# Kernel tuning notes

Hardware: AMD Instinct MI355X
Metric: run time of the kernel (lower is better)

Reference implementation:

```python
import jax, jax.numpy as jnp
import numpy as np

N_EMBD = 512
N_HEADS = 8
N_KV_HEADS = 2
HEAD_DIM = N_EMBD // N_HEADS  # 64
ROPE_BASE = 1000000.0
B, T = 2, 4096


def _rotate_half(x):
    h = x.shape[-1] // 2
    return jnp.concatenate([-x[..., h:], x[..., :h]], axis=-1)


def _build_rope(head_dim, seq_len, base, dtype):
    inv_freq = 1.0 / base ** (jnp.arange(0, head_dim, 2, dtype=jnp.float32) / head_dim)
    t = jnp.arange(seq_len, dtype=jnp.float32)
    freqs = jnp.outer(t, inv_freq)            # [T, head_dim/2]
    emb = jnp.concatenate([freqs, freqs], axis=-1)  # [T, head_dim]
    return emb.astype(dtype), None  # placeholder, cos/sin computed by caller


def setup_inputs() -> dict:
    key = jax.random.key(0)
    ks = jax.random.split(key, 8)
    s_in = 1.0 / np.sqrt(N_EMBD)
    x = jax.random.normal(ks[0], (B, T, N_EMBD), dtype=jnp.float32)
    Wq = jax.random.normal(ks[1], (N_EMBD, N_HEADS * HEAD_DIM), dtype=jnp.float32) * s_in
    bq = jnp.zeros((N_HEADS * HEAD_DIM,), dtype=jnp.float32)
    Wk = jax.random.normal(ks[2], (N_EMBD, N_KV_HEADS * HEAD_DIM), dtype=jnp.float32) * s_in
    bk = jnp.zeros((N_KV_HEADS * HEAD_DIM,), dtype=jnp.float32)
    Wv = jax.random.normal(ks[3], (N_EMBD, N_KV_HEADS * HEAD_DIM), dtype=jnp.float32) * s_in
    bv = jnp.zeros((N_KV_HEADS * HEAD_DIM,), dtype=jnp.float32)
    Wo = jax.random.normal(ks[4], (N_HEADS * HEAD_DIM, N_EMBD), dtype=jnp.float32) * s_in
    return {"x": x, "Wq": Wq, "bq": bq, "Wk": Wk, "bk": bk, "Wv": Wv, "bv": bv, "Wo": Wo}


def reference(x, Wq, bq, Wk, bk, Wv, bv, Wo):
    Bx, Tx, _ = x.shape
    scale = HEAD_DIM ** -0.5
    q = (x @ Wq + bq).reshape(Bx, Tx, N_HEADS, HEAD_DIM).transpose(0, 2, 1, 3)      # [B,H,T,D]
    k = (x @ Wk + bk).reshape(Bx, Tx, N_KV_HEADS, HEAD_DIM).transpose(0, 2, 1, 3)   # [B,Hkv,T,D]
    v = (x @ Wv + bv).reshape(Bx, Tx, N_KV_HEADS, HEAD_DIM).transpose(0, 2, 1, 3)

    # RoPE (built in fp32 then cast, matching torch impl)
    inv_freq = 1.0 / ROPE_BASE ** (jnp.arange(0, HEAD_DIM, 2, dtype=jnp.float32) / HEAD_DIM)
    t = jnp.arange(Tx, dtype=jnp.float32)
    freqs = jnp.outer(t, inv_freq)
    emb = jnp.concatenate([freqs, freqs], axis=-1)          # [T, D]
    cos = jnp.cos(emb).astype(x.dtype)[None, None, :, :]    # broadcast over B,H
    sin = jnp.sin(emb).astype(x.dtype)[None, None, :, :]
    q = q * cos + _rotate_half(q) * sin
    k = k * cos + _rotate_half(k) * sin

    rep = N_HEADS // N_KV_HEADS
    k = jnp.repeat(k, rep, axis=1)   # repeat_interleave on head dim
    v = jnp.repeat(v, rep, axis=1)

    attn = jnp.einsum("bhtd,bhsd->bhts", q, k) * scale      # [B,H,T,T]
    causal = jnp.tril(jnp.ones((Tx, Tx), dtype=bool))
    attn = jnp.where(causal, attn, jnp.finfo(attn.dtype).min)
    attn = jax.nn.softmax(attn, axis=-1)
    out = jnp.einsum("bhts,bhsd->bhtd", attn, v)            # [B,H,T,D]
    out = out.transpose(0, 2, 1, 3).reshape(Bx, Tx, N_HEADS * HEAD_DIM)
    return out @ Wo
```

## Files before the change

### kernel.cpp

```cpp
#include <hip/hip_runtime.h>

typedef unsigned short u16;
typedef unsigned int u32;
typedef __bf16 bf16x8_t __attribute__((ext_vector_type(8)));
typedef float f32x4_t __attribute__((ext_vector_type(4)));
typedef float f32x16_t __attribute__((ext_vector_type(16)));

#define T_SEQ 4096
#define EMB 512
#define NH 8
#define NKV 2
#define HD 64

__device__ __forceinline__ float bf2f(u16 h) {
    union { unsigned u; float f; } x; x.u = ((unsigned)h) << 16; return x.f;
}
__device__ __forceinline__ u16 f2bf(float f) {
    union { float f; unsigned u; } x; x.f = f;
    unsigned r = x.u + 0x7FFFu + ((x.u >> 16) & 1u);
    return (u16)(r >> 16);
}

__global__ __launch_bounds__(256)
void prep_kernel(const float* __restrict__ Wq, const float* __restrict__ Wk,
                 const float* __restrict__ Wv, const float* __restrict__ Wo,
                 u16* __restrict__ WqkvT, u16* __restrict__ WoT,
                 float* __restrict__ cost, float* __restrict__ sint)
{
    int i = blockIdx.x * 256 + threadIdx.x;
    if (i < 262144) {
        int n = i >> 9, k = i & 511;
        WqkvT[i] = f2bf(Wq[(size_t)k * 512 + n]);
    } else if (i < 327680) {
        int j = i - 262144;
        int n = j >> 9, k = j & 511;
        WqkvT[i] = f2bf(Wk[(size_t)k * 128 + n]);
    } else if (i < 393216) {
        int j = i - 327680;
        int n = j >> 9, k = j & 511;
        WqkvT[i] = f2bf(Wv[(size_t)k * 128 + n]);
    } else if (i < 655360) {
        int j = i - 393216;
        int n = j >> 9, k = j & 511;
        WoT[j] = f2bf(Wo[(size_t)k * 512 + n]);
    } else {
        int j = i - 655360;
        int t = j >> 5, jj = j & 31;
        double invf = pow(1.0e6, -(double)jj / 32.0);
        double ang = (double)t * invf;
        cost[j] = (float)cos(ang);
        sint[j] = (float)sin(ang);
    }
}

template <int EPI, int ASRC>
__global__ __launch_bounds__(256)
void gemm_kernel(const u16* __restrict__ A, const float* __restrict__ Af32,
                 const u16* __restrict__ Bt, int K,
                 float* __restrict__ C, int N,
                 const float* __restrict__ bq, const float* __restrict__ bk,
                 const float* __restrict__ bv,
                 const float* __restrict__ cost, const float* __restrict__ sint,
                 u16* __restrict__ qw, u16* __restrict__ kw, u16* __restrict__ vt)
{
    __shared__ __align__(16) u16 As[64][72];
    __shared__ __align__(16) u16 Bs[128][72];

    const int tid  = threadIdx.x;
    const int lane = tid & 63, wave = tid >> 6;
    const int wr = wave >> 1, wc = wave & 1;
    const int tm = blockIdx.x, tn = blockIdx.y;
    const int lrow = lane & 15, lgrp = lane >> 4;

    f32x4_t acc[2][4];
#pragma unroll
    for (int i = 0; i < 2; ++i)
#pragma unroll
        for (int j = 0; j < 4; ++j) acc[i][j] = (f32x4_t){0.f, 0.f, 0.f, 0.f};

    for (int k0 = 0; k0 < K; k0 += 64) {
        __syncthreads();
        {
            const int r0 = tid >> 3;
            const int ko = (tid & 7) * 8;
#pragma unroll
            for (int rr = 0; rr < 2; ++rr) {
                int row = r0 + rr * 32;
                int grow = tm * 64 + row;
                if (ASRC == 0) {
                    uint4 va = *reinterpret_cast<const uint4*>(A + (size_t)grow * K + k0 + ko);
                    *reinterpret_cast<uint4*>(&As[row][ko]) = va;
                } else {
                    float4 f0 = *reinterpret_cast<const float4*>(Af32 + (size_t)grow * K + k0 + ko);
                    float4 f1 = *reinterpret_cast<const float4*>(Af32 + (size_t)grow * K + k0 + ko + 4);
                    u16 o[8] = { f2bf(f0.x), f2bf(f0.y), f2bf(f0.z), f2bf(f0.w),
                                 f2bf(f1.x), f2bf(f1.y), f2bf(f1.z), f2bf(f1.w) };
                    *reinterpret_cast<uint4*>(&As[row][ko]) = *reinterpret_cast<uint4*>(o);
                }
            }
#pragma unroll
            for (int rr = 0; rr < 4; ++rr) {
                int row = r0 + rr * 32;
                uint4 vb = *reinterpret_cast<const uint4*>(Bt + (size_t)(tn * 128 + row) * K + k0 + ko);
                *reinterpret_cast<uint4*>(&Bs[row][ko]) = vb;
            }
        }
        __syncthreads();
#pragma unroll
        for (int kc = 0; kc < 2; ++kc) {
            bf16x8_t af[2], bf[4];
#pragma unroll
            for (int mb = 0; mb < 2; ++mb)
                af[mb] = *reinterpret_cast<const bf16x8_t*>(&As[wr * 32 + mb * 16 + lrow][kc * 32 + lgrp * 8]);
#pragma unroll
            for (int nb = 0; nb < 4; ++nb)
                bf[nb] = *reinterpret_cast<const bf16x8_t*>(&Bs[wc * 64 + nb * 16 + lrow][kc * 32 + lgrp * 8]);
#pragma unroll
            for (int mb = 0; mb < 2; ++mb)
#pragma unroll
                for (int nb = 0; nb < 4; ++nb)
                    acc[mb][nb] = __builtin_amdgcn_mfma_f32_16x16x32_bf16(af[mb], bf[nb], acc[mb][nb], 0, 0, 0);
        }
    }

    if (EPI == 0) {
#pragma unroll
        for (int mb = 0; mb < 2; ++mb)
#pragma unroll
            for (int nb = 0; nb < 4; ++nb)
#pragma unroll
                for (int r = 0; r < 4; ++r) {
                    int row = tm * 64 + wr * 32 + mb * 16 + lgrp * 4 + r;
                    int col = tn * 128 + wc * 64 + nb * 16 + lrow;
                    C[(size_t)row * N + col] = acc[mb][nb][r];
                }
    } else {
        const float QSC = 0.125f * 1.44269504088896f;
#pragma unroll
        for (int mb = 0; mb < 2; ++mb)
#pragma unroll
            for (int r = 0; r < 4; ++r) {
                int grow = tm * 64 + wr * 32 + mb * 16 + lgrp * 4 + r;
                int b = grow >> 12, t = grow & 4095;
#pragma unroll
                for (int nb = 0; nb < 2; ++nb) {
                    int n = tn * 128 + wc * 64 + nb * 16 + lrow;
                    int j = n & 63;
                    float c0 = acc[mb][nb][r];
                    float c1 = acc[mb][nb + 2][r];
                    if (n < 512) {
                        c0 += bq[n]; c1 += bq[n + 32];
                        float cs = cost[t * 32 + j], sn = sint[t * 32 + j];
                        float r0 = (c0 * cs - c1 * sn) * QSC;
                        float r1 = (c1 * cs + c0 * sn) * QSC;
                        int h = n >> 6;
                        size_t base = ((size_t)(b * NH + h) * T_SEQ + t) * HD;
                        qw[base + j]      = f2bf(r0);
                        qw[base + j + 32] = f2bf(r1);
                    } else if (n < 640) {
                        int nn = n - 512;
                        c0 += bk[nn]; c1 += bk[nn + 32];
                        float cs = cost[t * 32 + j], sn = sint[t * 32 + j];
                        float r0 = c0 * cs - c1 * sn;
                        float r1 = c1 * cs + c0 * sn;
                        int hk2 = nn >> 6;
                        size_t base = ((size_t)(b * NKV + hk2) * T_SEQ + t) * HD;
                        kw[base + j]      = f2bf(r0);
                        kw[base + j + 32] = f2bf(r1);
                    } else {
                        int nn = n - 640;
                        c0 += bv[nn]; c1 += bv[nn + 32];
                        int hv = nn >> 6;
                        size_t base = (size_t)(b * NKV + hv) * HD * T_SEQ;
                        vt[base + (size_t)j * T_SEQ + t]        = f2bf(c0);
                        vt[base + (size_t)(j + 32) * T_SEQ + t] = f2bf(c1);
                    }
                }
            }
    }
}

__global__ __launch_bounds__(256)
void attn_kernel(const u16* __restrict__ qw, const u16* __restrict__ kw,
                 const u16* __restrict__ vt, u16* __restrict__ po, float* __restrict__ lb)
{
    __shared__ __align__(16) u16 Ks[2][64][64];
    __shared__ __align__(16) u16 Vs[2][64][64];

    const int hdix = blockIdx.x;
    const int b = hdix >> 3, h = hdix & 7, hk = h >> 2;
    const int qt = 31 - (int)blockIdx.y;
    const int ck = blockIdx.z;
    const int tid = threadIdx.x, lane = tid & 63, wave = tid >> 6;
    const int lid = lane & 31, hi = lane >> 5;
    const int q0 = qt * 128 + wave * 32;
    const int kt0 = ck * (qt + 1);
    const int kt1 = kt0 + (qt + 1);

    const u16* kbase  = kw + (size_t)(b * NKV + hk) * T_SEQ * HD;
    const u16* vtbase = vt + (size_t)(b * NKV + hk) * HD * T_SEQ;

    const int ss = tid >> 3;
    const int sg = tid & 7;
    const int swz = (sg ^ (ss & 7)) << 3;

    bf16x8_t qf[4];
    {
        const u16* qrow = qw + ((size_t)(b * NH + h) * T_SEQ + q0 + lid) * HD + 8 * hi;
#pragma unroll
        for (int t = 0; t < 4; ++t)
            qf[t] = *reinterpret_cast<const bf16x8_t*>(qrow + 16 * t);
    }

    f32x16_t o0, o1, z16;
#pragma unroll
    for (int i = 0; i < 16; ++i) { o0[i] = 0.f; o1[i] = 0.f; z16[i] = 0.f; }
    const float M_FIX = 16.0f;
    float l = 0.f;

    {
        const int s2 = kt0 * 64;
        uint4 ka  = *reinterpret_cast<const uint4*>(kbase + (size_t)(s2 + ss) * HD + sg * 8);
        uint4 kb2 = *reinterpret_cast<const uint4*>(kbase + (size_t)(s2 + ss + 32) * HD + sg * 8);
        uint4 va  = *reinterpret_cast<const uint4*>(vtbase + (size_t)ss * T_SEQ + s2 + sg * 8);
        uint4 vb2 = *reinterpret_cast<const uint4*>(vtbase + (size_t)(ss + 32) * T_SEQ + s2 + sg * 8);
        *reinterpret_cast<uint4*>(&Ks[0][ss][swz]) = ka;
        *reinterpret_cast<uint4*>(&Ks[0][ss + 32][swz]) = kb2;
        *reinterpret_cast<uint4*>(&Vs[0][ss][swz]) = va;
        *reinterpret_cast<uint4*>(&Vs[0][ss + 32][swz]) = vb2;
    }
    __syncthreads();

    for (int kt = kt0; kt < kt1; ++kt) {
        const int cur = (kt - kt0) & 1, nxt = cur ^ 1;
        const bool pre = (kt + 1 < kt1);

        uint4 kr0, kr1, vr0, vr1;
        if (pre) {
            const int s2 = (kt + 1) * 64;
            kr0 = *reinterpret_cast<const uint4*>(kbase + (size_t)(s2 + ss) * HD + sg * 8);
            kr1 = *reinterpret_cast<const uint4*>(kbase + (size_t)(s2 + ss + 32) * HD + sg * 8);
            vr0 = *reinterpret_cast<const uint4*>(vtbase + (size_t)ss * T_SEQ + s2 + sg * 8);
            vr1 = *reinterpret_cast<const uint4*>(vtbase + (size_t)(ss + 32) * T_SEQ + s2 + sg * 8);
        }

        if (kt * 64 <= q0 + 31) {
            const bool full = (kt * 64 + 32 <= q0 + 31);
            const bool mreq = (kt * 64 + 63 > q0);

            f32x16_t s0, s1;
            __builtin_amdgcn_s_setprio(1);
#pragma unroll
            for (int t = 0; t < 4; ++t) {
                const int g = ((2 * t + hi) ^ (lid & 7)) << 3;
                bf16x8_t ka = *reinterpret_cast<const bf16x8_t*>(&Ks[cur][lid][g]);
                s0 = __builtin_amdgcn_mfma_f32_32x32x16_bf16(ka, qf[t], (t == 0) ? z16 : s0, 0, 0, 0);
                if (full) {
                    bf16x8_t kb2 = *reinterpret_cast<const bf16x8_t*>(&Ks[cur][lid + 32][g]);
                    s1 = __builtin_amdgcn_mfma_f32_32x32x16_bf16(kb2, qf[t], (t == 0) ? z16 : s1, 0, 0, 0);
                }
            }
            __builtin_amdgcn_s_setprio(0);

            if (mreq) {
                const int qg = q0 + lid;
                const int kvb = kt * 64 + 4 * hi;
#pragma unroll
                for (int r = 0; r < 16; ++r) {
                    int kv = kvb + (r & 3) + 8 * (r >> 2);
                    if (kv > qg) s0[r] = -1e30f;
                    if (full && kv + 32 > qg) s1[r] = -1e30f;
                }
            }

#pragma unroll
            for (int r = 0; r < 16; ++r) s0[r] = exp2f(s0[r] - M_FIX);
            if (full) {
#pragma unroll
                for (int r = 0; r < 16; ++r) s1[r] = exp2f(s1[r] - M_FIX);
            }

            {
                float rs = 0.f;
#pragma unroll
                for (int q4 = 0; q4 < 4; ++q4)
                    rs += (s0[4 * q4] + s0[4 * q4 + 1]) + (s0[4 * q4 + 2] + s0[4 * q4 + 3]);
                if (full) {
#pragma unroll
                    for (int q4 = 0; q4 < 4; ++q4)
                        rs += (s1[4 * q4] + s1[4 * q4 + 1]) + (s1[4 * q4 + 2] + s1[4 * q4 + 3]);
                }
                rs += __shfl_xor(rs, 32);
                l += rs;
            }

            bf16x8_t pa[4];
            {
                u32 pw[8];
#pragma unroll
                for (int c = 0; c < 4; ++c) {
                    asm("v_cvt_pk_bf16_f32 %0, %1, %2" : "=v"(pw[2 * c])     : "v"(s0[4 * c]),     "v"(s0[4 * c + 1]));
                    asm("v_cvt_pk_bf16_f32 %0, %1, %2" : "=v"(pw[2 * c + 1]) : "v"(s0[4 * c + 2]), "v"(s0[4 * c + 3]));
                }
                asm("v_permlane32_swap_b32 %0, %1" : "+v"(pw[0]), "+v"(pw[2]));
                asm("v_permlane32_swap_b32 %0, %1" : "+v"(pw[1]), "+v"(pw[3]));
                asm("v_permlane32_swap_b32 %0, %1" : "+v"(pw[4]), "+v"(pw[6]));
                asm("v_permlane32_swap_b32 %0, %1" : "+v"(pw[5]), "+v"(pw[7]));
                uint4 f0 = {pw[0], pw[1], pw[2], pw[3]};
                uint4 f1 = {pw[4], pw[5], pw[6], pw[7]};
                pa[0] = __builtin_bit_cast(bf16x8_t, f0);
                pa[1] = __builtin_bit_cast(bf16x8_t, f1);
                if (full) {
#pragma unroll
                    for (int c = 0; c < 4; ++c) {
                        asm("v_cvt_pk_bf16_f32 %0, %1, %2" : "=v"(pw[2 * c])     : "v"(s1[4 * c]),     "v"(s1[4 * c + 1]));
                        asm("v_cvt_pk_bf16_f32 %0, %1, %2" : "=v"(pw[2 * c + 1]) : "v"(s1[4 * c + 2]), "v"(s1[4 * c + 3]));
                    }
                    asm("v_permlane32_swap_b32 %0, %1" : "+v"(pw[0]), "+v"(pw[2]));
                    asm("v_permlane32_swap_b32 %0, %1" : "+v"(pw[1]), "+v"(pw[3]));
                    asm("v_permlane32_swap_b32 %0, %1" : "+v"(pw[4]), "+v"(pw[6]));
                    asm("v_permlane32_swap_b32 %0, %1" : "+v"(pw[5]), "+v"(pw[7]));
                    uint4 g0 = {pw[0], pw[1], pw[2], pw[3]};
                    uint4 g1 = {pw[4], pw[5], pw[6], pw[7]};
                    pa[2] = __builtin_bit_cast(bf16x8_t, g0);
                    pa[3] = __builtin_bit_cast(bf16x8_t, g1);
                }
            }

            __builtin_amdgcn_s_setprio(1);
            const int ns = full ? 4 : 2;
#pragma unroll
            for (int s = 0; s < 4; ++s) {
                if (s >= ns) break;
                const int g = ((2 * s + hi) ^ (lid & 7)) << 3;
                bf16x8_t v0f = *reinterpret_cast<const bf16x8_t*>(&Vs[cur][lid][g]);
                bf16x8_t v1f = *reinterpret_cast<const bf16x8_t*>(&Vs[cur][lid + 32][g]);
                o0 = __builtin_amdgcn_mfma_f32_32x32x16_bf16(pa[s], v0f, o0, 0, 0, 0);
                o1 = __builtin_amdgcn_mfma_f32_32x32x16_bf16(pa[s], v1f, o1, 0, 0, 0);
            }
            __builtin_amdgcn_s_setprio(0);
        }

        if (pre) {
            *reinterpret_cast<uint4*>(&Ks[nxt][ss][swz]) = kr0;
            *reinterpret_cast<uint4*>(&Ks[nxt][ss + 32][swz]) = kr1;
            *reinterpret_cast<uint4*>(&Vs[nxt][ss][swz]) = vr0;
            *reinterpret_cast<uint4*>(&Vs[nxt][ss + 32][swz]) = vr1;
            __syncthreads();
        }
    }

    {
        u16* pob = po + (size_t)ck * 4194304;
        const int rowb = (hdix * 32 + qt) * 128;
#pragma unroll
        for (int r = 0; r < 16; ++r) {
            int qr = (r & 3) + 8 * (r >> 2) + 4 * hi;
            size_t base = (size_t)(rowb + wave * 32 + qr) * HD;
            pob[base + lid]      = f2bf(o0[r]);
            pob[base + lid + 32] = f2bf(o1[r]);
        }
        if (hi == 0)
            lb[(size_t)ck * 65536 + rowb + wave * 32 + lid] = l;
    }
}

__global__ __launch_bounds__(256)
void combine_kernel(const u16* __restrict__ po, const float* __restrict__ lb,
                    u16* __restrict__ ao)
{
    int id = blockIdx.x * 256 + threadIdx.x;
    int row = id >> 3, oct = id & 7;
    int bhqt = row >> 7, qrow = row & 127;
    int bh = bhqt >> 5, qt = bhqt & 31;
    int b = bh >> 3, h = bh & 7;
    int t = qt * 128 + qrow;

    float inv = 1.0f / (lb[row] + lb[65536 + row]);
    const u16* p0 = po + (size_t)row * HD + oct * 8;
    const u16* p1 = p0 + 4194304;
    uint4 a = *reinterpret_cast<const uint4*>(p0);
    uint4 c = *reinterpret_cast<const uint4*>(p1);
    const u16* pa = reinterpret_cast<const u16*>(&a);
    const u16* pc = reinterpret_cast<const u16*>(&c);
    u16 outv[8];
#pragma unroll
    for (int j = 0; j < 8; ++j)
        outv[j] = f2bf((bf2f(pa[j]) + bf2f(pc[j])) * inv);
    size_t base = ((size_t)(b * T_SEQ) + t) * EMB + h * HD + oct * 8;
    *reinterpret_cast<uint2*>(ao + base)     = *reinterpret_cast<uint2*>(&outv[0]);
    *reinterpret_cast<uint2*>(ao + base + 4) = *reinterpret_cast<uint2*>(&outv[4]);
}

extern "C" void kernel_launch(void* const* d_in, const int* in_sizes, int n_in,
                              void* d_out, int out_size, void* d_ws, size_t ws_size,
                              hipStream_t stream)
{
    const float* x  = (const float*)d_in[0];
    const float* Wq = (const float*)d_in[1];
    const float* bq = (const float*)d_in[2];
    const float* Wk = (const float*)d_in[3];
    const float* bk = (const float*)d_in[4];
    const float* Wv = (const float*)d_in[5];
    const float* bv = (const float*)d_in[6];
    const float* Wo = (const float*)d_in[7];
    float* out = (float*)d_out;

    char* ws = (char*)d_ws;
    u16*   WqkvT = (u16*)(ws);
    u16*   WoT   = (u16*)(ws + 786432);
    float* cost  = (float*)(ws + 1310720);
    float* sint  = (float*)(ws + 1835008);
    u16*   qw    = (u16*)(ws + 10747904);
    u16*   kw    = (u16*)(ws + 19136512);
    u16*   vt    = (u16*)(ws + 21233664);
    u16*   ao    = (u16*)(ws + 23330816);
    u16*   po    = (u16*)(ws + 31719424);
    float* lb    = (float*)(ws + 48496640);

    prep_kernel<<<3072, 256, 0, stream>>>(Wq, Wk, Wv, Wo, WqkvT, WoT, cost, sint);

    dim3 gp(128, 6);
    gemm_kernel<1, 1><<<gp, 256, 0, stream>>>(nullptr, x, WqkvT, 512,
                                              nullptr, 768,
                                              bq, bk, bv, cost, sint, qw, kw, vt);

    dim3 ga(2 * NH, 32, 2);
    attn_kernel<<<ga, 256, 0, stream>>>(qw, kw, vt, po, lb);

    combine_kernel<<<65536 * 8 / 256, 256, 0, stream>>>(po, lb, ao);

    dim3 go(128, 4);
    gemm_kernel<0, 0><<<go, 256, 0, stream>>>(ao, nullptr, WoT, 512,
                                              out, 512,
                                              nullptr, nullptr, nullptr, nullptr, nullptr,
                                              nullptr, nullptr, nullptr);
}
```

Before: 130.7 us.

## Fuse split-K attention combine into attention kernel via atomic last-block reduction

Removes the separate combine kernel. Each attention block now bumps an atomic counter for its query tile, and the second of the two key-split blocks to finish merges the other block's partial output and normalizer with its own register accumulators, then writes the final bf16 output. The grid is also flattened to 1D so the two splits of a tile sit next to each other in launch order. This saves one kernel launch and a round trip of reading the partial outputs, at the cost of threadfences and an atomic per block, plus counters that are zeroed in the prep kernel.

```diff
diff --git a/kernel.cpp b/kernel.cpp
--- a/kernel.cpp
+++ b/kernel.cpp
@@ -25,7 +25,7 @@
 void prep_kernel(const float* __restrict__ Wq, const float* __restrict__ Wk,
                  const float* __restrict__ Wv, const float* __restrict__ Wo,
                  u16* __restrict__ WqkvT, u16* __restrict__ WoT,
-                 float* __restrict__ cost, float* __restrict__ sint)
+                 float* __restrict__ cost, float* __restrict__ sint, int* __restrict__ cnt)
 {
     int i = blockIdx.x * 256 + threadIdx.x;
     if (i < 262144) {
@@ -43,13 +43,15 @@
         int j = i - 393216;
         int n = j >> 9, k = j & 511;
         WoT[j] = f2bf(Wo[(size_t)k * 512 + n]);
-    } else {
+    } else if (i < 786432) {
         int j = i - 655360;
         int t = j >> 5, jj = j & 31;
         double invf = pow(1.0e6, -(double)jj / 32.0);
         double ang = (double)t * invf;
         cost[j] = (float)cos(ang);
         sint[j] = (float)sin(ang);
+    } else {
+        cnt[i - 786432] = 0;
     }
 }
 
@@ -182,15 +184,18 @@
 
 __global__ __launch_bounds__(256)
 void attn_kernel(const u16* __restrict__ qw, const u16* __restrict__ kw,
-                 const u16* __restrict__ vt, u16* __restrict__ po, float* __restrict__ lb)
+                 const u16* __restrict__ vt, u16* __restrict__ po, float* __restrict__ lb,
+                 int* __restrict__ cnt, u16* __restrict__ ao)
 {
     __shared__ __align__(16) u16 Ks[2][64][64];
     __shared__ __align__(16) u16 Vs[2][64][64];
-
-    const int hdix = blockIdx.x;
+    __shared__ int flag;
+
+    const int gid = blockIdx.x;
+    const int hdix = gid & 15;
+    const int ck = (gid >> 4) & 1;
+    const int qt = 31 - (gid >> 5);
     const int b = hdix >> 3, h = hdix & 7, hk = h >> 2;
-    const int qt = 31 - (int)blockIdx.y;
-    const int ck = blockIdx.z;
     const int tid = threadIdx.x, lane = tid & 63, wave = tid >> 6;
     const int lid = lane & 31, hi = lane >> 5;
     const int q0 = qt * 128 + wave * 32;
@@ -350,9 +355,9 @@
         }
     }
 
+    const int rowb = (hdix * 32 + qt) * 128;
     {
         u16* pob = po + (size_t)ck * 4194304;
-        const int rowb = (hdix * 32 + qt) * 128;
 #pragma unroll
         for (int r = 0; r < 16; ++r) {
             int qr = (r & 3) + 8 * (r >> 2) + 4 * hi;
@@ -363,33 +368,26 @@
         if (hi == 0)
             lb[(size_t)ck * 65536 + rowb + wave * 32 + lid] = l;
     }
-}
-
-__global__ __launch_bounds__(256)
-void combine_kernel(const u16* __restrict__ po, const float* __restrict__ lb,
-                    u16* __restrict__ ao)
-{
-    int id = blockIdx.x * 256 + threadIdx.x;
-    int row = id >> 3, oct = id & 7;
-    int bhqt = row >> 7, qrow = row & 127;
-    int bh = bhqt >> 5, qt = bhqt & 31;
-    int b = bh >> 3, h = bh & 7;
-    int t = qt * 128 + qrow;
-
-    float inv = 1.0f / (lb[row] + lb[65536 + row]);
-    const u16* p0 = po + (size_t)row * HD + oct * 8;
-    const u16* p1 = p0 + 4194304;
-    uint4 a = *reinterpret_cast<const uint4*>(p0);
-    uint4 c = *reinterpret_cast<const uint4*>(p1);
-    const u16* pa = reinterpret_cast<const u16*>(&a);
-    const u16* pc = reinterpret_cast<const u16*>(&c);
-    u16 outv[8];
-#pragma unroll
-    for (int j = 0; j < 8; ++j)
-        outv[j] = f2bf((bf2f(pa[j]) + bf2f(pc[j])) * inv);
-    size_t base = ((size_t)(b * T_SEQ) + t) * EMB + h * HD + oct * 8;
-    *reinterpret_cast<uint2*>(ao + base)     = *reinterpret_cast<uint2*>(&outv[0]);
-    *reinterpret_cast<uint2*>(ao + base + 4) = *reinterpret_cast<uint2*>(&outv[4]);
+    __threadfence();
+    if (tid == 0) flag = atomicAdd(&cnt[hdix * 32 + qt], 1);
+    __syncthreads();
+    if (flag == 1) {
+        __threadfence();
+        const int ock = ck ^ 1;
+        const u16* pob2 = po + (size_t)ock * 4194304;
+        float lo = lb[(size_t)ock * 65536 + rowb + wave * 32 + lid];
+        float inv = 1.0f / (l + lo);
+#pragma unroll
+        for (int r = 0; r < 16; ++r) {
+            int qr = (r & 3) + 8 * (r >> 2) + 4 * hi;
+            float ir = __shfl(inv, qr);
+            size_t pbase = (size_t)(rowb + wave * 32 + qr) * HD;
+            int t = qt * 128 + wave * 32 + qr;
+            size_t abase = ((size_t)(b * T_SEQ) + t) * EMB + h * HD;
+            ao[abase + lid]      = f2bf((o0[r] + bf2f(pob2[pbase + lid]))      * ir);
+            ao[abase + lid + 32] = f2bf((o1[r] + bf2f(pob2[pbase + lid + 32])) * ir);
+        }
+    }
 }
 
 extern "C" void kernel_launch(void* const* d_in, const int* in_sizes, int n_in,
@@ -417,18 +415,16 @@
     u16*   ao    = (u16*)(ws + 23330816);
     u16*   po    = (u16*)(ws + 31719424);
     float* lb    = (float*)(ws + 48496640);
-
-    prep_kernel<<<3072, 256, 0, stream>>>(Wq, Wk, Wv, Wo, WqkvT, WoT, cost, sint);
+    int*   cnt   = (int*)(ws + 49020928);
+
+    prep_kernel<<<3074, 256, 0, stream>>>(Wq, Wk, Wv, Wo, WqkvT, WoT, cost, sint, cnt);
 
     dim3 gp(128, 6);
     gemm_kernel<1, 1><<<gp, 256, 0, stream>>>(nullptr, x, WqkvT, 512,
                                               nullptr, 768,
                                               bq, bk, bv, cost, sint, qw, kw, vt);
 
-    dim3 ga(2 * NH, 32, 2);
-    attn_kernel<<<ga, 256, 0, stream>>>(qw, kw, vt, po, lb);
-
-    combine_kernel<<<65536 * 8 / 256, 256, 0, stream>>>(po, lb, ao);
+    attn_kernel<<<1024, 256, 0, stream>>>(qw, kw, vt, po, lb, cnt, ao);
 
     dim3 go(128, 4);
     gemm_kernel<0, 0><<<go, 256, 0, stream>>>(ao, nullptr, WoT, 512,
```

New measurement: 281.2 us. +115.2%, slower.
